# Kernel tuning notes

Hardware: AMD Instinct MI355X
Metric: run time of the kernel (lower is better)

Reference implementation:

```python
import jax, jax.numpy as jnp
import numpy as np

N_NODES, C, R, L, H, NB = 50000, 512, 4096, 32, 4, 4  # NB blocks: enc0, enc1, pma, dec0
LN_EPS = 1e-5

def _layer_norm(x, g, b):
    mu = jnp.mean(x, axis=-1, keepdims=True)
    var = jnp.var(x, axis=-1, keepdims=True)
    return (x - mu) * jax.lax.rsqrt(var + LN_EPS) * g + b

def _mab(x, y, y_mask, x_mask, Wq, bq, Wk, bk, Wv, bv, Wo, bo, ffW, ffb, g1, b1, g2, b2):
    # Multihead attention block (SetTransformer MAB), dropout=0 at inference.
    Rr, Lq, Cc = x.shape
    Lk = y.shape[1]
    Dh = Cc // H
    q = (x @ Wq.T + bq).reshape(Rr, Lq, H, Dh)
    k = (y @ Wk.T + bk).reshape(Rr, Lk, H, Dh)
    v = (y @ Wv.T + bv).reshape(Rr, Lk, H, Dh)
    scores = jnp.einsum('rqhd,rkhd->rhqk', q, k) * (1.0 / Dh ** 0.5)
    if y_mask is not None:  # mask padded keys (ragged gene sets)
        scores = jnp.where(y_mask[:, None, None, :], scores, jnp.float32(-1e30))
    attn = jax.nn.softmax(scores, axis=-1)
    out = jnp.einsum('rhqk,rkhd->rqhd', attn, v).reshape(Rr, Lq, Cc)
    out = out @ Wo.T + bo
    if x_mask is not None:  # zero attention output at padded query rows
        out = jnp.where(x_mask[..., None], out, 0.0)
    out = _layer_norm(out + x, g1, b1)
    out = _layer_norm(out + jax.nn.relu(out @ ffW.T + ffb), g2, b2)
    return out

def setup_inputs() -> dict:
    key = jax.random.key(0)
    ks = jax.random.split(key, 10)
    s = 0.02
    return {
        'gene_embeddings': jax.random.normal(ks[0], (N_NODES, C), jnp.float32),
        'reaction_gene_idx': jax.random.randint(ks[1], (R, L), 0, N_NODES),
        'reaction_lengths': jax.random.randint(ks[2], (R,), 1, L + 1),
        'Wq': jax.random.normal(ks[3], (NB, C, C), jnp.float32) * s,
        'Wk': jax.random.normal(ks[4], (NB, C, C), jnp.float32) * s,
        'Wv': jax.random.normal(ks[5], (NB, C, C), jnp.float32) * s,
        'Wo': jax.random.normal(ks[6], (NB, C, C), jnp.float32) * s,
        'ffW': jax.random.normal(ks[7], (NB, C, C), jnp.float32) * s,
        'bq': jnp.zeros((NB, C), jnp.float32),
        'bk': jnp.zeros((NB, C), jnp.float32),
        'bv': jnp.zeros((NB, C), jnp.float32),
        'bo': jnp.zeros((NB, C), jnp.float32),
        'ffb': jnp.zeros((NB, C), jnp.float32),
        'g1': jnp.ones((NB, C), jnp.float32),
        'b1': jnp.zeros((NB, C), jnp.float32),
        'g2': jnp.ones((NB, C), jnp.float32),
        'b2': jnp.zeros((NB, C), jnp.float32),
        'pma_lin_W': jax.random.normal(ks[8], (C, C), jnp.float32) * s,
        'pma_lin_b': jnp.zeros((C,), jnp.float32),
        'seed': jax.random.normal(ks[9], (1, C), jnp.float32) * s,
    }

def reference(gene_embeddings, reaction_gene_idx, reaction_lengths, Wq, Wk, Wv, Wo, ffW, bq, bk, bv, bo, ffb, g1, b1, g2, b2, pma_lin_W, pma_lin_b, seed):
    mask = jnp.arange(L)[None, :] < reaction_lengths[:, None]  # [R, L] ragged validity mask
    x = gene_embeddings[reaction_gene_idx]                     # [R, L, C] per-reaction gather
    x = jnp.where(mask[..., None], x, 0.0)
    def blk(i, xq, ykv, ymask, xmask):
        return _mab(xq, ykv, ymask, xmask, Wq[i], bq[i], Wk[i], bk[i], Wv[i], bv[i],
                    Wo[i], bo[i], ffW[i], ffb[i], g1[i], b1[i], g2[i], b2[i])
    x = blk(0, x, x, mask, mask)   # encoder SAB 0
    x = blk(1, x, x, mask, mask)   # encoder SAB 1
    y = jax.nn.relu(x @ pma_lin_W.T + pma_lin_b)
    sd = jnp.broadcast_to(seed[None, :, :], (R, 1, C))
    x = blk(2, sd, y, mask, None)  # PMA: 1 seed attends over gene set
    x = blk(3, x, x, None, None)   # decoder SAB over the single seed
    out = jnp.mean(x, axis=1)      # [R, C] (1 seed, concat=False)
    out = jnp.where((reaction_lengths > 0)[:, None], out, 0.0)  # empty reactions -> zeros
    return out
```

## Files before the change

kernel.cpp:

```cpp
#include <hip/hip_runtime.h>
#include <stdint.h>

#define R_ 4096
#define L_ 32
#define C_ 512
#define H_ 4
#define DH_ 128

typedef __bf16 bf16x8 __attribute__((ext_vector_type(8)));
typedef float f32x4 __attribute__((ext_vector_type(4)));

__device__ __forceinline__ float b2f(unsigned int u) {
    union { unsigned int i; float f; } x; x.i = u << 16; return x.f;
}
__device__ __forceinline__ unsigned short f2b(float f) {
    union { float f; unsigned int i; } x; x.f = f;
    unsigned int i = x.i;
    i += 0x7fffu + ((i >> 16) & 1u);
    return (unsigned short)(i >> 16);
}
__device__ __forceinline__ void unpack8(uint4 v, float* x) {
    x[0] = b2f(v.x & 0xffffu); x[1] = b2f(v.x >> 16);
    x[2] = b2f(v.y & 0xffffu); x[3] = b2f(v.y >> 16);
    x[4] = b2f(v.z & 0xffffu); x[5] = b2f(v.z >> 16);
    x[6] = b2f(v.w & 0xffffu); x[7] = b2f(v.w >> 16);
}
__device__ __forceinline__ uint4 pack8(const float* x) {
    uint4 v;
    v.x = (unsigned)f2b(x[0]) | ((unsigned)f2b(x[1]) << 16);
    v.y = (unsigned)f2b(x[2]) | ((unsigned)f2b(x[3]) << 16);
    v.z = (unsigned)f2b(x[4]) | ((unsigned)f2b(x[5]) << 16);
    v.w = (unsigned)f2b(x[6]) | ((unsigned)f2b(x[7]) << 16);
    return v;
}

__device__ __forceinline__ void gload_lds16(const unsigned short* g, unsigned short* l) {
    __builtin_amdgcn_global_load_lds(
        (const __attribute__((address_space(1))) void*)g,
        (__attribute__((address_space(3))) void*)l, 16, 0, 0);
}

__global__ __launch_bounds__(256)
void detect_kernel(const unsigned short* __restrict__ gene, int* __restrict__ flag) {
    __shared__ int cnt;
    if (threadIdx.x == 0) cnt = 0;
    __syncthreads();
    int local = 0;
    for (int j = 0; j < 8; ++j) {
        int i = threadIdx.x * 8 + j;
        unsigned short u = gene[2 * i];
        int e = (u >> 7) & 0xFF;
        if (e >= 100 && e <= 140) ++local;
    }
    atomicAdd(&cnt, local);
    __syncthreads();
    if (threadIdx.x == 0) *flag = (cnt >= 1024) ? 1 : 0;
}

__global__ __launch_bounds__(256)
void cvt_any_kernel(const void* __restrict__ in, unsigned short* __restrict__ out,
                    int n, const int* __restrict__ flag, int src_off) {
    int i0 = (blockIdx.x * 256 + threadIdx.x) * 8;
    if (i0 >= n) return;
    if (*flag) {
        *(uint4*)(out + i0) = *(const uint4*)((const unsigned short*)in + src_off + i0);
    } else {
        const float* f = (const float*)in + src_off;
        float4 a = *(const float4*)(f + i0);
        float4 b = *(const float4*)(f + i0 + 4);
        float x[8] = {a.x, a.y, a.z, a.w, b.x, b.y, b.z, b.w};
        *(uint4*)(out + i0) = pack8(x);
    }
}

__global__ __launch_bounds__(256)
void bias_concat_kernel(const unsigned short* __restrict__ bq, const unsigned short* __restrict__ bk,
                        const unsigned short* __restrict__ bv,
                        unsigned short* __restrict__ bqkv0, unsigned short* __restrict__ bqkv1,
                        unsigned short* __restrict__ bkv2) {
    int t = threadIdx.x;
#pragma unroll
    for (int s = 0; s < 2; ++s) {
        int i = t + s * 256;
        bqkv0[i]        = bq[i];
        bqkv0[i + 512]  = bk[i];
        bqkv0[i + 1024] = bv[i];
        bqkv1[i]        = bq[i + 512];
        bqkv1[i + 512]  = bk[i + 512];
        bqkv1[i + 1024] = bv[i + 512];
        bkv2[i]         = bk[i + 1024];
        bkv2[i + 512]   = bv[i + 1024];
    }
}

__global__ __launch_bounds__(256)
void qp_kernel(const unsigned short* __restrict__ Wq2, const unsigned short* __restrict__ bq2,
               const unsigned short* __restrict__ seed, unsigned short* __restrict__ qp) {
    __shared__ float sv[512];
    int t = threadIdx.x;
    sv[t] = b2f(seed[t]); sv[t + 256] = b2f(seed[t + 256]);
    __syncthreads();
#pragma unroll
    for (int s = 0; s < 2; ++s) {
        int n = t + s * 256;
        const unsigned short* wrow = Wq2 + (size_t)n * 512;
        float acc = 0.f;
        for (int k8 = 0; k8 < 64; ++k8) {
            float x[8];
            unpack8(*(const uint4*)(wrow + k8 * 8), x);
#pragma unroll
            for (int e = 0; e < 8; ++e) acc += x[e] * sv[k8 * 8 + e];
        }
        qp[n] = f2b(acc + b2f(bq2[n]));
    }
}

__global__ __launch_bounds__(256)
void diag_kernel(unsigned short* __restrict__ out, int n, float val) {
    int i = blockIdx.x * 256 + threadIdx.x;
    if (i < n) out[i] = f2b(val);
}

__global__ __launch_bounds__(256)
void scan_kernel(const int* __restrict__ lens, int* __restrict__ off,
                 int* __restrict__ meta, int Rc) {
    __shared__ int tsum[257];
    const int t = threadIdx.x;
    const int chunk = (Rc + 255) / 256;
    const int lo = t * chunk;
    const int hi = min(lo + chunk, Rc);
    int s = 0;
    for (int i = lo; i < hi; ++i) {
        int l = lens[i]; l = max(0, min(32, l));
        s += l;
    }
    tsum[t] = s;
    __syncthreads();
    if (t == 0) {
        int acc = 0;
        for (int i = 0; i < 256; ++i) { int v = tsum[i]; tsum[i] = acc; acc += v; }
        tsum[256] = acc;
        meta[0] = acc;
        meta[1] = (acc + 127) & ~127;
    }
    __syncthreads();
    int run = tsum[t];
    for (int i = lo; i < hi; ++i) {
        off[i] = run;
        int l = lens[i]; l = max(0, min(32, l));
        run += l;
    }
}

__global__ __launch_bounds__(256)
void gather_kernel(const void* __restrict__ gene_v, const int* __restrict__ gidx,
                   const int* __restrict__ lens, const int* __restrict__ off,
                   unsigned short* __restrict__ X, const int* __restrict__ flag) {
    int tid = blockIdx.x * 256 + threadIdx.x;
    int m = tid >> 6;
    int ch = tid & 63;
    int r = m >> 5, j = m & 31;
    if (j >= lens[r]) return;
    size_t dst = (size_t)(off[r] + j) * C_ + ch * 8;
    size_t base = (size_t)gidx[m] * C_ + ch * 8;
    uint4 v;
    if (*flag) {
        v = *(const uint4*)((const unsigned short*)gene_v + base);
    } else {
        const float* f = (const float*)gene_v;
        float4 a = *(const float4*)(f + base);
        float4 b = *(const float4*)(f + base + 4);
        float x[8] = {a.x, a.y, a.z, a.w, b.x, b.y, b.z, b.w};
        v = pack8(x);
    }
    *(uint4*)(X + dst) = v;
}

__global__ __launch_bounds__(256)
void ztail_kernel(unsigned short* __restrict__ X, const int* __restrict__ meta) {
    int tid = blockIdx.x * 256 + threadIdx.x;
    int m = meta[0] + (tid >> 6);
    int ch = tid & 63;
    if (m < meta[1])
        *(uint4*)(X + (size_t)m * C_ + ch * 8) = make_uint4(0u, 0u, 0u, 0u);
}

__global__ __launch_bounds__(256)
void seed_kernel(const unsigned short* __restrict__ seed, unsigned short* __restrict__ Xs) {
    int i = blockIdx.x * 256 + threadIdx.x;
    int ch = i & 63;
    uint4 v = *(const uint4*)(seed + ch * 8);
    *(uint4*)(Xs + (size_t)i * 8) = v;
}

__global__ __launch_bounds__(256)
void final_kernel(const unsigned short* __restrict__ S, const int* __restrict__ lens,
                  void* __restrict__ out, const int* __restrict__ flag, size_t elem_off) {
    int i = blockIdx.x * 256 + threadIdx.x;
    int r = i >> 6;
    uint4 v = make_uint4(0u, 0u, 0u, 0u);
    if (lens[r] > 0) v = *(const uint4*)(S + (size_t)i * 8);
    if (*flag) {
        *(uint4*)((unsigned short*)out + elem_off + (size_t)i * 8) = v;
    } else {
        float x[8];
        unpack8(v, x);
        float* o = (float*)out + elem_off + (size_t)i * 8;
        *(float4*)o       = make_float4(x[0], x[1], x[2], x[3]);
        *(float4*)(o + 4) = make_float4(x[4], x[5], x[6], x[7]);
    }
}

template<int NT>
__global__ __launch_bounds__(256, 2)
void gemm_bt_kernel(const unsigned short* __restrict__ A, const unsigned short* __restrict__ W,
                    const unsigned short* __restrict__ bias, unsigned short* __restrict__ Out,
                    int relu, const int* __restrict__ meta, int MT) {
    const int b = blockIdx.x;
    const int xcd = b & 7;
    const int j = b >> 3;
    const int ml = j / NT;
    const int n = j - ml * NT;
    const int m = ml * 8 + xcd;
    if (m >= MT) return;
    const int m0 = m * 128, n0 = n * 256;
    if (meta && m0 >= meta[1]) return;
    const int ldo = NT * 256;

    __shared__ unsigned short As[128 * 64];
    __shared__ unsigned short Bs[256 * 64];

    const int t = threadIdx.x;
    const int wave = t >> 6, lane = t & 63;
    const int quad = lane >> 4, lr = lane & 15;
    const int wr = wave >> 1, wc = wave & 1;

    const int srow8 = lane >> 3;
    const int scol8 = (lane & 7) ^ srow8;
    const unsigned short* gaB = A + (size_t)(m0 + wave * 8 + srow8) * C_ + scol8 * 8;
    const unsigned short* gbB = W + (size_t)(n0 + wave * 8 + srow8) * C_ + scol8 * 8;
    unsigned short* lA = As + wave * 512;
    unsigned short* lB = Bs + wave * 512;

    f32x4 acc[4][8] = {};

    for (int k0 = 0; k0 < C_; k0 += 64) {
        __syncthreads();
#pragma unroll
        for (int jj = 0; jj < 4; ++jj)
            gload_lds16(gaB + (size_t)jj * 32 * C_ + k0, lA + jj * 2048);
#pragma unroll
        for (int jj = 0; jj < 8; ++jj)
            gload_lds16(gbB + (size_t)jj * 32 * C_ + k0, lB + jj * 2048);
        __syncthreads();

#pragma unroll
        for (int kk = 0; kk < 2; ++kk) {
            bf16x8 af[4], bfr[8];
#pragma unroll
            for (int i = 0; i < 4; ++i)
                af[i] = *(const bf16x8*)&As[(64 * wr + 16 * i + lr) * 64 +
                                            (((kk << 2) + quad) ^ (lr & 7)) * 8];
#pragma unroll
            for (int jj = 0; jj < 8; ++jj)
                bfr[jj] = *(const bf16x8*)&Bs[(128 * wc + 16 * jj + lr) * 64 +
                                              (((kk << 2) + quad) ^ (lr & 7)) * 8];
#pragma unroll
            for (int i = 0; i < 4; ++i)
#pragma unroll
                for (int jj = 0; jj < 8; ++jj)
                    acc[i][jj] = __builtin_amdgcn_mfma_f32_16x16x32_bf16(af[i], bfr[jj], acc[i][jj], 0, 0, 0);
        }
    }

#pragma unroll
    for (int i = 0; i < 4; ++i) {
        int row = m0 + 64 * wr + 16 * i + quad * 4;
#pragma unroll
        for (int jj = 0; jj < 8; ++jj) {
            int col = n0 + 128 * wc + 16 * jj + lr;
            float bv = b2f(bias[col]);
#pragma unroll
            for (int r = 0; r < 4; ++r) {
                float v = acc[i][jj][r] + bv;
                if (relu) v = fmaxf(v, 0.f);
                Out[(size_t)(row + r) * ldo + col] = f2b(v);
            }
        }
    }
}

template<int NK>
__device__ __forceinline__ void attn_enc_body(
    const unsigned short* __restrict__ QKV, unsigned short* __restrict__ O,
    int h, int t, int len, int base,
    unsigned short* Qs, unsigned short* Ks, float (*Sc)[33]) {

#pragma unroll
    for (int it = 0; it < NK; ++it) {
        int flat = t + it * 128;
        int row = flat >> 4, ch = flat & 15;
        if (row < len) {
            size_t g = ((size_t)(base + row)) * 1536 + h * DH_ + ch * 8;
            *(uint4*)&Qs[row * 136 + ch * 8] = *(const uint4*)(QKV + g);
            *(uint4*)&Ks[row * 136 + ch * 8] = *(const uint4*)(QKV + g + 512);
        }
    }
    __syncthreads();

    const unsigned* Qw = (const unsigned*)Qs;
    const unsigned* Kw = (const unsigned*)Ks;

    {
        const int qg = t >> 3, kg = t & 7;
        float aqk[2][NK];
#pragma unroll
        for (int j = 0; j < 2; ++j)
#pragma unroll
            for (int i = 0; i < NK; ++i) aqk[j][i] = 0.f;
        for (int d2 = 0; d2 < 64; ++d2) {
            unsigned q0 = Qw[qg * 68 + d2];
            unsigned q1 = Qw[(qg + 16) * 68 + d2];
            float q0l = b2f(q0 & 0xffffu), q0h = b2f(q0 >> 16);
            float q1l = b2f(q1 & 0xffffu), q1h = b2f(q1 >> 16);
#pragma unroll
            for (int i = 0; i < NK; ++i) {
                unsigned kv = Kw[(kg + 8 * i) * 68 + d2];
                float kl = b2f(kv & 0xffffu), kh = b2f(kv >> 16);
                aqk[0][i] += q0l * kl + q0h * kh;
                aqk[1][i] += q1l * kl + q1h * kh;
            }
        }
        const float scale = 0.08838834764831845f;
#pragma unroll
        for (int j = 0; j < 2; ++j)
#pragma unroll
            for (int i = 0; i < NK; ++i) {
                int k = kg + 8 * i;
                Sc[qg + 16 * j][k] = (k < len) ? aqk[j][i] * scale : -1e30f;
            }
    }
    __syncthreads();

    if (t < len) {
        float mx = -3e38f;
        for (int k = 0; k < len; ++k) mx = fmaxf(mx, Sc[t][k]);
        float sum = 0.f;
        for (int k = 0; k < len; ++k) { float e = __expf(Sc[t][k] - mx); Sc[t][k] = e; sum += e; }
        float inv = 1.f / sum;
        for (int k = 0; k < len; ++k) Sc[t][k] *= inv;
    }
    __syncthreads();

    {
        const int qh = t >> 3, g = t & 7;
        float av[2][16] = {};
        const unsigned short* Vg = QKV + (size_t)base * 1536 + 1024 + h * DH_ + g * 8;
        for (int k = 0; k < len; ++k) {
            float a0 = Sc[qh][k], a1 = Sc[qh + 16][k];
            const unsigned short* vrow = Vg + (size_t)k * 1536;
            float v0[8], v1[8];
            unpack8(*(const uint4*)vrow, v0);
            unpack8(*(const uint4*)(vrow + 64), v1);
#pragma unroll
            for (int e = 0; e < 8; ++e) {
                av[0][e]     += a0 * v0[e];
                av[0][8 + e] += a0 * v1[e];
                av[1][e]     += a1 * v0[e];
                av[1][8 + e] += a1 * v1[e];
            }
        }
#pragma unroll
        for (int qi = 0; qi < 2; ++qi) {
            int q = qh + 16 * qi;
            if (q >= len) continue;
            size_t ga = ((size_t)(base + q)) * C_ + h * DH_;
#pragma unroll
            for (int j = 0; j < 2; ++j) {
                float tmp[8];
#pragma unroll
                for (int e = 0; e < 8; ++e) tmp[e] = av[qi][j * 8 + e];
                *(uint4*)(O + ga + g * 8 + 64 * j) = pack8(tmp);
            }
        }
    }
}

__global__ __launch_bounds__(128)
void attn_enc_kernel(const unsigned short* __restrict__ QKV, unsigned short* __restrict__ O,
                     const int* __restrict__ lens, const int* __restrict__ off) {
    const int r = blockIdx.x, h = blockIdx.y, t = threadIdx.x;
    const int len = lens[r];
    if (len <= 0) return;
    const int base = off[r];
    __shared__ unsigned short Qs[32 * 136], Ks[32 * 136];
    __shared__ float Sc[32][33];
    switch ((len + 7) >> 3) {
        case 1:  attn_enc_body<1>(QKV, O, h, t, len, base, Qs, Ks, Sc); break;
        case 2:  attn_enc_body<2>(QKV, O, h, t, len, base, Qs, Ks, Sc); break;
        case 3:  attn_enc_body<3>(QKV, O, h, t, len, base, Qs, Ks, Sc); break;
        default: attn_enc_body<4>(QKV, O, h, t, len, base, Qs, Ks, Sc); break;
    }
}

__global__ __launch_bounds__(64)
void attn_pma_kernel(const unsigned short* __restrict__ qp, const unsigned short* __restrict__ KV,
                     unsigned short* __restrict__ O,
                     const int* __restrict__ lens, const int* __restrict__ off) {
    const int r = blockIdx.x, h = blockIdx.y, t = threadIdx.x;
    const int len = lens[r];
    if (len <= 0) return;
    const int base = off[r];
    __shared__ float qv[128];
    __shared__ float attn[32];
    const size_t qb = (size_t)r * C_ + h * DH_;
    qv[t]      = b2f(qp[h * DH_ + t]);
    qv[t + 64] = b2f(qp[h * DH_ + t + 64]);
    __syncthreads();
    if (t < 32 && t < len) {
        const unsigned short* krow = KV + ((size_t)(base + t)) * 1024 + h * DH_;
        float s = 0.f;
        for (int d = 0; d < 128; ++d) s += qv[d] * b2f(krow[d]);
        attn[t] = s * 0.08838834764831845f;
    }
    __syncthreads();
    if (t == 0) {
        float mx = -3e38f;
        for (int k = 0; k < len; ++k) mx = fmaxf(mx, attn[k]);
        float sum = 0.f;
        for (int k = 0; k < len; ++k) { float e = __expf(attn[k] - mx); attn[k] = e; sum += e; }
        float inv = 1.f / sum;
        for (int k = 0; k < len; ++k) attn[k] *= inv;
    }
    __syncthreads();
    float a0 = 0.f, a1 = 0.f;
    for (int k = 0; k < len; ++k) {
        const unsigned short* vrow = KV + ((size_t)(base + k)) * 1024 + 512 + h * DH_;
        float a = attn[k];
        a0 += a * b2f(vrow[t]);
        a1 += a * b2f(vrow[t + 64]);
    }
    O[qb + t]      = f2b(a0);
    O[qb + t + 64] = f2b(a1);
}

__global__ __launch_bounds__(256)
void ln_kernel(const unsigned short* __restrict__ A, const unsigned short* __restrict__ Res,
               const unsigned short* __restrict__ gamma, const unsigned short* __restrict__ beta,
               unsigned short* __restrict__ out, const int* __restrict__ lens, int use_mask,
               const int* __restrict__ meta) {
    const int m = blockIdx.x * 4 + (threadIdx.x >> 6);
    if (meta && m >= meta[1]) return;
    const int lane = threadIdx.x & 63;
    const bool masked = use_mask && ((m & 31) >= lens[m >> 5]);
    const size_t base = (size_t)m * C_ + lane * 8;
    float xa[8], xr[8], x[8];
    unpack8(*(const uint4*)(A + base), xa);
    unpack8(*(const uint4*)(Res + base), xr);
    float s = 0.f, ss = 0.f;
#pragma unroll
    for (int e = 0; e < 8; ++e) {
        x[e] = (masked ? 0.f : xa[e]) + xr[e];
        s += x[e]; ss += x[e] * x[e];
    }
#pragma unroll
    for (int off = 32; off > 0; off >>= 1) {
        s  += __shfl_down(s, off);
        ss += __shfl_down(ss, off);
    }
    s = __shfl(s, 0); ss = __shfl(ss, 0);
    const float mu = s * (1.f / 512.f);
    const float rinv = rsqrtf(fmaxf(ss * (1.f / 512.f) - mu * mu, 0.f) + 1e-5f);
    float gg[8], bb[8], y[8];
    unpack8(*(const uint4*)(gamma + lane * 8), gg);
    unpack8(*(const uint4*)(beta + lane * 8), bb);
#pragma unroll
    for (int e = 0; e < 8; ++e) y[e] = (x[e] - mu) * rinv * gg[e] + bb[e];
    *(uint4*)(out + base) = pack8(y);
}

extern "C" void kernel_launch(void* const* d_in, const int* in_sizes, int n_in,
                              void* d_out, int out_size, void* d_ws, size_t ws_size,
                              hipStream_t stream) {
    (void)in_sizes; (void)n_in;
    const void* gene = d_in[0];
    const int*  gidx = (const int*)d_in[1];
    const int*  lens = (const int*)d_in[2];

    int* ibase = (int*)d_ws;
    int* flag  = ibase;
    int* meta  = ibase + 2;
    int* d_off = ibase + 8;
    unsigned short* ws0 = (unsigned short*)(ibase + 8 + 4096);
    const size_t hdr_bytes = (size_t)(8 + 4096) * 4;

    size_t off = 0;
    auto take = [&](size_t elems) { unsigned short* p = ws0 + off; off += elems; return p; };
    const size_t CC = (size_t)C_ * C_;
    unsigned short* wEnc0 = take(3 * CC);
    unsigned short* wEnc1 = take(3 * CC);
    unsigned short* wKVp  = take(2 * CC);
    unsigned short* wO  = take(4 * CC);
    unsigned short* wF  = take(4 * CC);
    unsigned short* wP  = take(CC);
    unsigned short* wQp = take(CC);
    unsigned short* wVd = take(CC);
    unsigned short* cbq = take(4 * C_);
    unsigned short* cbk = take(4 * C_);
    unsigned short* cbv = take(4 * C_);
    unsigned short* cbo = take(4 * C_);
    unsigned short* cff = take(4 * C_);
    unsigned short* cg1 = take(4 * C_);
    unsigned short* cb1 = take(4 * C_);
    unsigned short* cg2 = take(4 * C_);
    unsigned short* cb2 = take(4 * C_);
    unsigned short* cpb = take(C_);
    unsigned short* csd = take(C_);
    unsigned short* bqkv0 = take(3 * C_);
    unsigned short* bqkv1 = take(3 * C_);
    unsigned short* bkv2  = take(2 * C_);
    unsigned short* qp    = take(C_);
    const size_t wbytes = hdr_bytes + off * 2;

    const size_t per_r = ((size_t)32 * 2560 + 4 * 512) * 2;
    int Rc = 0;
    const int cands[6] = {4096, 2048, 1024, 512, 256, 128};
    for (int i = 0; i < 6; ++i) {
        size_t need = wbytes + (size_t)cands[i] * per_r;
        if (need <= ws_size) { Rc = cands[i]; break; }
    }
    if (Rc == 0) {
        diag_kernel<<<(out_size + 255) / 256, 256, 0, stream>>>(
            (unsigned short*)d_out, out_size, 1000.0f + (float)(ws_size >> 20));
        return;
    }
    const int Mc = Rc * 32;

    unsigned short* X    = take((size_t)Mc * C_);
    unsigned short* AQKV = take((size_t)Mc * 1536);
    unsigned short* Aout = take((size_t)Mc * C_);
    unsigned short* S0 = take((size_t)Rc * C_);
    unsigned short* S1 = take((size_t)Rc * C_);
    unsigned short* S2 = take((size_t)Rc * C_);
    unsigned short* S3 = take((size_t)Rc * C_);

    detect_kernel<<<1, 256, 0, stream>>>((const unsigned short*)gene, flag);
    auto cvt = [&](const void* in, unsigned short* out_, int n, int src_off) {
        cvt_any_kernel<<<(n + 2047) / 2048, 256, 0, stream>>>(in, out_, n, flag, src_off);
    };
    cvt(d_in[3], wEnc0,          (int)CC, 0);
    cvt(d_in[4], wEnc0 + CC,     (int)CC, 0);
    cvt(d_in[5], wEnc0 + 2 * CC, (int)CC, 0);
    cvt(d_in[3], wEnc1,          (int)CC, (int)CC);
    cvt(d_in[4], wEnc1 + CC,     (int)CC, (int)CC);
    cvt(d_in[5], wEnc1 + 2 * CC, (int)CC, (int)CC);
    cvt(d_in[4], wKVp,      (int)CC, (int)(2 * CC));
    cvt(d_in[5], wKVp + CC, (int)CC, (int)(2 * CC));
    cvt(d_in[3], wQp, (int)CC, (int)(2 * CC));
    cvt(d_in[5], wVd, (int)CC, (int)(3 * CC));
    cvt(d_in[6], wO, (int)(4 * CC), 0);
    cvt(d_in[7], wF, (int)(4 * CC), 0);
    cvt(d_in[17], wP, (int)CC, 0);
    cvt(d_in[8],  cbq, 4 * C_, 0); cvt(d_in[9],  cbk, 4 * C_, 0); cvt(d_in[10], cbv, 4 * C_, 0);
    cvt(d_in[11], cbo, 4 * C_, 0); cvt(d_in[12], cff, 4 * C_, 0);
    cvt(d_in[13], cg1, 4 * C_, 0); cvt(d_in[14], cb1, 4 * C_, 0);
    cvt(d_in[15], cg2, 4 * C_, 0); cvt(d_in[16], cb2, 4 * C_, 0);
    cvt(d_in[18], cpb, C_, 0);     cvt(d_in[19], csd, C_, 0);
    bias_concat_kernel<<<1, 256, 0, stream>>>(cbq, cbk, cbv, bqkv0, bqkv1, bkv2);
    qp_kernel<<<1, 256, 0, stream>>>(wQp, cbq + 2 * C_, csd, qp);

    auto gemm = [&](auto nt_tag, const unsigned short* Ain, const unsigned short* Win,
                    const unsigned short* bias, unsigned short* Outp, int Mrows, int relu,
                    const int* mt) {
        constexpr int NT = decltype(nt_tag)::value;
        const int MT = Mrows / 128;
        const int grid = 8 * ((MT + 7) / 8) * NT;
        gemm_bt_kernel<NT><<<dim3(grid), 256, 0, stream>>>(Ain, Win, bias, Outp, relu, mt, MT);
    };
    using N2 = std::integral_constant<int, 2>;
    using N4 = std::integral_constant<int, 4>;
    using N6 = std::integral_constant<int, 6>;

    for (int c = 0; c < R_ / Rc; ++c) {
        const int r0 = c * Rc;
        const int* lc = lens + r0;

        scan_kernel<<<1, 256, 0, stream>>>(lc, d_off, meta, Rc);
        gather_kernel<<<Mc * 64 / 256, 256, 0, stream>>>(
            gene, gidx + (size_t)r0 * L_, lc, d_off, X, flag);
        ztail_kernel<<<32, 256, 0, stream>>>(X, meta);

        for (int i = 0; i < 2; ++i) {
            gemm(N6{}, X, i ? wEnc1 : wEnc0, i ? bqkv1 : bqkv0, AQKV, Mc, 0, meta);
            attn_enc_kernel<<<dim3(Rc, H_), 128, 0, stream>>>(AQKV, Aout, lc, d_off);
            gemm(N2{}, Aout, wO + (size_t)i * CC, cbo + i * C_, AQKV, Mc, 0, meta);
            ln_kernel<<<Mc / 4, 256, 0, stream>>>(AQKV, X, cg1 + i * C_, cb1 + i * C_, X, lc, 0, meta);
            gemm(N2{}, X, wF + (size_t)i * CC, cff + i * C_, Aout, Mc, 1, meta);
            ln_kernel<<<Mc / 4, 256, 0, stream>>>(Aout, X, cg2 + i * C_, cb2 + i * C_, X, lc, 0, meta);
        }

        gemm(N2{}, X, wP, cpb, Aout, Mc, 1, meta);
        seed_kernel<<<Rc * 64 / 256, 256, 0, stream>>>(csd, S0);

        {
            gemm(N4{}, Aout, wKVp, bkv2, AQKV, Mc, 0, meta);
            attn_pma_kernel<<<dim3(Rc, H_), 64, 0, stream>>>(qp, AQKV, S2, lc, d_off);
            gemm(N2{}, S2, wO + 2 * CC, cbo + 2 * C_, S3, Rc, 0, nullptr);
            ln_kernel<<<Rc / 4, 256, 0, stream>>>(S3, S0, cg1 + 2 * C_, cb1 + 2 * C_, S0, lc, 0, nullptr);
            gemm(N2{}, S0, wF + 2 * CC, cff + 2 * C_, S1, Rc, 1, nullptr);
            ln_kernel<<<Rc / 4, 256, 0, stream>>>(S1, S0, cg2 + 2 * C_, cb2 + 2 * C_, S0, lc, 0, nullptr);
        }

        {
            gemm(N2{}, S0, wVd, cbv + 3 * C_, S1, Rc, 0, nullptr);
            gemm(N2{}, S1, wO + 3 * CC, cbo + 3 * C_, S2, Rc, 0, nullptr);
            ln_kernel<<<Rc / 4, 256, 0, stream>>>(S2, S0, cg1 + 3 * C_, cb1 + 3 * C_, S0, lc, 0, nullptr);
            gemm(N2{}, S0, wF + 3 * CC, cff + 3 * C_, S1, Rc, 1, nullptr);
            ln_kernel<<<Rc / 4, 256, 0, stream>>>(S1, S0, cg2 + 3 * C_, cb2 + 3 * C_, S0, lc, 0, nullptr);
        }

        final_kernel<<<Rc * 64 / 256, 256, 0, stream>>>(S0, lc, d_out, flag, (size_t)r0 * C_);
    }
}
```

Before: 1.917 ms.

## Fold PMA K/V projections into attention and merge decoder Wv·Wo weights

The PMA block no longer runs the K/V projection GEMM over all gene rows. The fixed seed query is folded into Wk to give a per-head vector for scoring, and Wv is applied after attention pooling, inside the attention kernel. In the decoder, the Wv and Wo projections are pre-multiplied into a single matrix with a combined bias, which removes one GEMM. Encoder QK^T scores now use bf16 MFMA instructions instead of scalar FMA. The risks are extra rounding from the bf16 combined weights, and scalar per-row matvecs in the PMA kernel that may not use compute well.

```diff
diff --git a/kernel.cpp b/kernel.cpp
--- a/kernel.cpp
+++ b/kernel.cpp
@@ -76,8 +76,7 @@
 __global__ __launch_bounds__(256)
 void bias_concat_kernel(const unsigned short* __restrict__ bq, const unsigned short* __restrict__ bk,
                         const unsigned short* __restrict__ bv,
-                        unsigned short* __restrict__ bqkv0, unsigned short* __restrict__ bqkv1,
-                        unsigned short* __restrict__ bkv2) {
+                        unsigned short* __restrict__ bqkv0, unsigned short* __restrict__ bqkv1) {
     int t = threadIdx.x;
 #pragma unroll
     for (int s = 0; s < 2; ++s) {
@@ -88,8 +87,6 @@
         bqkv1[i]        = bq[i + 512];
         bqkv1[i + 512]  = bk[i + 512];
         bqkv1[i + 1024] = bv[i + 512];
-        bkv2[i]         = bk[i + 1024];
-        bkv2[i + 512]   = bv[i + 1024];
     }
 }
 
@@ -113,6 +110,63 @@
         }
         qp[n] = f2b(acc + b2f(bq2[n]));
     }
+}
+
+__global__ __launch_bounds__(256)
+void wkq_kernel(const unsigned short* __restrict__ Wk2, const unsigned short* __restrict__ qp,
+                float* __restrict__ wkq) {
+    const int h = blockIdx.x, t = threadIdx.x;
+    __shared__ float qv[128];
+    if (t < 128) qv[t] = b2f(qp[h * 128 + t]);
+    __syncthreads();
+    float a0 = 0.f, a1 = 0.f;
+    for (int j = 0; j < 128; ++j) {
+        const unsigned short* row = Wk2 + (size_t)(h * 128 + j) * 512;
+        float q = qv[j];
+        a0 += q * b2f(row[t]);
+        a1 += q * b2f(row[t + 256]);
+    }
+    const float scale = 0.08838834764831845f;
+    wkq[h * 512 + t]       = a0 * scale;
+    wkq[h * 512 + t + 256] = a1 * scale;
+}
+
+__global__ __launch_bounds__(256)
+void wc_kernel(const unsigned short* __restrict__ Wo3, const unsigned short* __restrict__ Wv3,
+               unsigned short* __restrict__ Wc) {
+    const int i = blockIdx.x, t = threadIdx.x;
+    __shared__ float wo[512];
+    wo[t] = b2f(Wo3[(size_t)i * 512 + t]);
+    wo[t + 256] = b2f(Wo3[(size_t)i * 512 + t + 256]);
+    __syncthreads();
+    float a0 = 0.f, a1 = 0.f;
+    for (int d = 0; d < 512; ++d) {
+        const unsigned short* row = Wv3 + (size_t)d * 512;
+        float w = wo[d];
+        a0 += w * b2f(row[t]);
+        a1 += w * b2f(row[t + 256]);
+    }
+    Wc[(size_t)i * 512 + t]       = f2b(a0);
+    Wc[(size_t)i * 512 + t + 256] = f2b(a1);
+}
+
+__global__ __launch_bounds__(256)
+void bc_kernel(const unsigned short* __restrict__ Wo3, const unsigned short* __restrict__ bv3,
+               const unsigned short* __restrict__ bo3, unsigned short* __restrict__ bc) {
+    const int t = threadIdx.x;
+    __shared__ float bvv[512];
+    bvv[t] = b2f(bv3[t]); bvv[t + 256] = b2f(bv3[t + 256]);
+    __syncthreads();
+    const int i = blockIdx.x * 256 + t;
+    const unsigned short* row = Wo3 + (size_t)i * 512;
+    float acc = 0.f;
+    for (int d8 = 0; d8 < 64; ++d8) {
+        float x[8];
+        unpack8(*(const uint4*)(row + d8 * 8), x);
+#pragma unroll
+        for (int e = 0; e < 8; ++e) acc += x[e] * bvv[d8 * 8 + e];
+    }
+    bc[i] = f2b(acc + b2f(bo3[i]));
 }
 
 __global__ __launch_bounds__(256)
@@ -308,37 +362,29 @@
     }
     __syncthreads();
 
-    const unsigned* Qw = (const unsigned*)Qs;
-    const unsigned* Kw = (const unsigned*)Ks;
-
     {
-        const int qg = t >> 3, kg = t & 7;
-        float aqk[2][NK];
-#pragma unroll
-        for (int j = 0; j < 2; ++j)
-#pragma unroll
-            for (int i = 0; i < NK; ++i) aqk[j][i] = 0.f;
-        for (int d2 = 0; d2 < 64; ++d2) {
-            unsigned q0 = Qw[qg * 68 + d2];
-            unsigned q1 = Qw[(qg + 16) * 68 + d2];
-            float q0l = b2f(q0 & 0xffffu), q0h = b2f(q0 >> 16);
-            float q1l = b2f(q1 & 0xffffu), q1h = b2f(q1 >> 16);
-#pragma unroll
-            for (int i = 0; i < NK; ++i) {
-                unsigned kv = Kw[(kg + 8 * i) * 68 + d2];
-                float kl = b2f(kv & 0xffffu), kh = b2f(kv >> 16);
-                aqk[0][i] += q0l * kl + q0h * kh;
-                aqk[1][i] += q1l * kl + q1h * kh;
+        const int wv = t >> 6;
+        const int ln_ = t & 63;
+        const int quad = ln_ >> 4, lr = ln_ & 15;
+        f32x4 a0 = {0.f, 0.f, 0.f, 0.f};
+        f32x4 a1 = {0.f, 0.f, 0.f, 0.f};
+#pragma unroll
+        for (int s = 0; s < 4; ++s) {
+            bf16x8 aq = *(const bf16x8*)&Qs[(wv * 16 + lr) * 136 + s * 32 + quad * 8];
+            bf16x8 k0 = *(const bf16x8*)&Ks[lr * 136 + s * 32 + quad * 8];
+            a0 = __builtin_amdgcn_mfma_f32_16x16x32_bf16(aq, k0, a0, 0, 0, 0);
+            if (NK >= 3) {
+                bf16x8 k1 = *(const bf16x8*)&Ks[(16 + lr) * 136 + s * 32 + quad * 8];
+                a1 = __builtin_amdgcn_mfma_f32_16x16x32_bf16(aq, k1, a1, 0, 0, 0);
             }
         }
         const float scale = 0.08838834764831845f;
 #pragma unroll
-        for (int j = 0; j < 2; ++j)
-#pragma unroll
-            for (int i = 0; i < NK; ++i) {
-                int k = kg + 8 * i;
-                Sc[qg + 16 * j][k] = (k < len) ? aqk[j][i] * scale : -1e30f;
-            }
+        for (int reg = 0; reg < 4; ++reg) {
+            int q = wv * 16 + quad * 4 + reg;
+            Sc[q][lr] = a0[reg] * scale;
+            if (NK >= 3) Sc[q][16 + lr] = a1[reg] * scale;
+        }
     }
     __syncthreads();
 
@@ -404,24 +450,27 @@
 }
 
 __global__ __launch_bounds__(64)
-void attn_pma_kernel(const unsigned short* __restrict__ qp, const unsigned short* __restrict__ KV,
+void attn_pma_kernel(const float* __restrict__ wkq, const unsigned short* __restrict__ Y,
+                     const unsigned short* __restrict__ Wv, const unsigned short* __restrict__ bv,
                      unsigned short* __restrict__ O,
                      const int* __restrict__ lens, const int* __restrict__ off) {
     const int r = blockIdx.x, h = blockIdx.y, t = threadIdx.x;
     const int len = lens[r];
     if (len <= 0) return;
     const int base = off[r];
-    __shared__ float qv[128];
     __shared__ float attn[32];
-    const size_t qb = (size_t)r * C_ + h * DH_;
-    qv[t]      = b2f(qp[h * DH_ + t]);
-    qv[t + 64] = b2f(qp[h * DH_ + t + 64]);
-    __syncthreads();
+    __shared__ float sv[512];
     if (t < 32 && t < len) {
-        const unsigned short* krow = KV + ((size_t)(base + t)) * 1024 + h * DH_;
+        const unsigned short* yrow = Y + (size_t)(base + t) * C_;
+        const float* wk = wkq + h * 512;
         float s = 0.f;
-        for (int d = 0; d < 128; ++d) s += qv[d] * b2f(krow[d]);
-        attn[t] = s * 0.08838834764831845f;
+        for (int d8 = 0; d8 < 64; ++d8) {
+            float x[8];
+            unpack8(*(const uint4*)(yrow + d8 * 8), x);
+#pragma unroll
+            for (int e = 0; e < 8; ++e) s += x[e] * wk[d8 * 8 + e];
+        }
+        attn[t] = s;
     }
     __syncthreads();
     if (t == 0) {
@@ -433,15 +482,32 @@
         for (int k = 0; k < len; ++k) attn[k] *= inv;
     }
     __syncthreads();
-    float a0 = 0.f, a1 = 0.f;
-    for (int k = 0; k < len; ++k) {
-        const unsigned short* vrow = KV + ((size_t)(base + k)) * 1024 + 512 + h * DH_;
-        float a = attn[k];
-        a0 += a * b2f(vrow[t]);
-        a1 += a * b2f(vrow[t + 64]);
-    }
-    O[qb + t]      = f2b(a0);
-    O[qb + t + 64] = f2b(a1);
+    {
+        float acc[8] = {};
+        for (int k = 0; k < len; ++k) {
+            float a = attn[k];
+            float x[8];
+            unpack8(*(const uint4*)(Y + (size_t)(base + k) * C_ + t * 8), x);
+#pragma unroll
+            for (int e = 0; e < 8; ++e) acc[e] += a * x[e];
+        }
+#pragma unroll
+        for (int e = 0; e < 8; ++e) sv[t * 8 + e] = acc[e];
+    }
+    __syncthreads();
+#pragma unroll
+    for (int jj = 0; jj < 2; ++jj) {
+        int jcol = t + jj * 64;
+        const unsigned short* wrow = Wv + (size_t)(h * 128 + jcol) * C_;
+        float s = 0.f;
+        for (int d8 = 0; d8 < 64; ++d8) {
+            float x[8];
+            unpack8(*(const uint4*)(wrow + d8 * 8), x);
+#pragma unroll
+            for (int e = 0; e < 8; ++e) s += x[e] * sv[d8 * 8 + e];
+        }
+        O[(size_t)r * C_ + h * 128 + jcol] = f2b(s + b2f(bv[h * 128 + jcol]));
+    }
 }
 
 __global__ __launch_bounds__(256)
@@ -491,20 +557,23 @@
     int* flag  = ibase;
     int* meta  = ibase + 2;
     int* d_off = ibase + 8;
-    unsigned short* ws0 = (unsigned short*)(ibase + 8 + 4096);
-    const size_t hdr_bytes = (size_t)(8 + 4096) * 4;
+    float* wkq = (float*)(ibase + 8 + 4096);
+    unsigned short* ws0 = (unsigned short*)(ibase + 8 + 4096 + 2048);
+    const size_t hdr_bytes = (size_t)(8 + 4096 + 2048) * 4;
 
     size_t off = 0;
     auto take = [&](size_t elems) { unsigned short* p = ws0 + off; off += elems; return p; };
     const size_t CC = (size_t)C_ * C_;
     unsigned short* wEnc0 = take(3 * CC);
     unsigned short* wEnc1 = take(3 * CC);
-    unsigned short* wKVp  = take(2 * CC);
+    unsigned short* wKp = take(CC);
+    unsigned short* wVp = take(CC);
     unsigned short* wO  = take(4 * CC);
     unsigned short* wF  = take(4 * CC);
     unsigned short* wP  = take(CC);
     unsigned short* wQp = take(CC);
     unsigned short* wVd = take(CC);
+    unsigned short* wWc = take(CC);
     unsigned short* cbq = take(4 * C_);
     unsigned short* cbk = take(4 * C_);
     unsigned short* cbv = take(4 * C_);
@@ -518,7 +587,7 @@
     unsigned short* csd = take(C_);
     unsigned short* bqkv0 = take(3 * C_);
     unsigned short* bqkv1 = take(3 * C_);
-    unsigned short* bkv2  = take(2 * C_);
+    unsigned short* bcb   = take(C_);
     unsigned short* qp    = take(C_);
     const size_t wbytes = hdr_bytes + off * 2;
 
@@ -554,8 +623,8 @@
     cvt(d_in[3], wEnc1,          (int)CC, (int)CC);
     cvt(d_in[4], wEnc1 + CC,     (int)CC, (int)CC);
     cvt(d_in[5], wEnc1 + 2 * CC, (int)CC, (int)CC);
-    cvt(d_in[4], wKVp,      (int)CC, (int)(2 * CC));
-    cvt(d_in[5], wKVp + CC, (int)CC, (int)(2 * CC));
+    cvt(d_in[4], wKp, (int)CC, (int)(2 * CC));
+    cvt(d_in[5], wVp, (int)CC, (int)(2 * CC));
     cvt(d_in[3], wQp, (int)CC, (int)(2 * CC));
     cvt(d_in[5], wVd, (int)CC, (int)(3 * CC));
     cvt(d_in[6], wO, (int)(4 * CC), 0);
@@ -566,8 +635,11 @@
     cvt(d_in[13], cg1, 4 * C_, 0); cvt(d_in[14], cb1, 4 * C_, 0);
     cvt(d_in[15], cg2, 4 * C_, 0); cvt(d_in[16], cb2, 4 * C_, 0);
     cvt(d_in[18], cpb, C_, 0);     cvt(d_in[19], csd, C_, 0);
-    bias_concat_kernel<<<1, 256, 0, stream>>>(cbq, cbk, cbv, bqkv0, bqkv1, bkv2);
+    bias_concat_kernel<<<1, 256, 0, stream>>>(cbq, cbk, cbv, bqkv0, bqkv1);
     qp_kernel<<<1, 256, 0, stream>>>(wQp, cbq + 2 * C_, csd, qp);
+    wkq_kernel<<<4, 256, 0, stream>>>(wKp, qp, wkq);
+    wc_kernel<<<512, 256, 0, stream>>>(wO + 3 * CC, wVd, wWc);
+    bc_kernel<<<2, 256, 0, stream>>>(wO + 3 * CC, cbv + 3 * C_, cbo + 3 * C_, bcb);
 
     auto gemm = [&](auto nt_tag, const unsigned short* Ain, const unsigned short* Win,
                     const unsigned short* bias, unsigned short* Outp, int Mrows, int relu,
@@ -578,7 +650,6 @@
         gemm_bt_kernel<NT><<<dim3(grid), 256, 0, stream>>>(Ain, Win, bias, Outp, relu, mt, MT);
     };
     using N2 = std::integral_constant<int, 2>;
-    using N4 = std::integral_constant<int, 4>;
     using N6 = std::integral_constant<int, 6>;
 
     for (int c = 0; c < R_ / Rc; ++c) {
@@ -603,8 +674,7 @@
         seed_kernel<<<Rc * 64 / 256, 256, 0, stream>>>(csd, S0);
 
         {
-            gemm(N4{}, Aout, wKVp, bkv2, AQKV, Mc, 0, meta);
-            attn_pma_kernel<<<dim3(Rc, H_), 64, 0, stream>>>(qp, AQKV, S2, lc, d_off);
+            attn_pma_kernel<<<dim3(Rc, H_), 64, 0, stream>>>(wkq, Aout, wVp, cbv + 2 * C_, S2, lc, d_off);
             gemm(N2{}, S2, wO + 2 * CC, cbo + 2 * C_, S3, Rc, 0, nullptr);
             ln_kernel<<<Rc / 4, 256, 0, stream>>>(S3, S0, cg1 + 2 * C_, cb1 + 2 * C_, S0, lc, 0, nullptr);
             gemm(N2{}, S0, wF + 2 * CC, cff + 2 * C_, S1, Rc, 1, nullptr);
@@ -612,8 +682,7 @@
         }
 
         {
-            gemm(N2{}, S0, wVd, cbv + 3 * C_, S1, Rc, 0, nullptr);
-            gemm(N2{}, S1, wO + 3 * CC, cbo + 3 * C_, S2, Rc, 0, nullptr);
+            gemm(N2{}, S0, wWc, bcb, S2, Rc, 0, nullptr);
             ln_kernel<<<Rc / 4, 256, 0, stream>>>(S2, S0, cg1 + 3 * C_, cb1 + 3 * C_, S0, lc, 0, nullptr);
             gemm(N2{}, S0, wF + 3 * CC, cff + 3 * C_, S1, Rc, 1, nullptr);
             ln_kernel<<<Rc / 4, 256, 0, stream>>>(S1, S0, cg2 + 3 * C_, cb2 + 3 * C_, S0, lc, 0, nullptr);
```

New measurement: 1.959 ms. 2.2% more time.
